# Kernel optimization log

Measured on AMD Instinct MI355X. Metric: run time of the kernel, lower is better.

The kernel has to match this reference:

```python
import jax, jax.numpy as jnp
import numpy as np

N_NODES = 50000
N_EDGES = 800000
EDGE_F = 96
NODE_F = 256
GLOB_F = 64
HIDDEN = 1024
N_GRAPHS = 8
MLP_IN = NODE_F + 3 * EDGE_F + GLOB_F  # 608


def setup_inputs() -> dict:
    key = jax.random.key(0)
    ks = jax.random.split(key, 9)
    x = jax.random.normal(ks[0], (N_NODES, NODE_F), dtype=jnp.float32)
    edge_attr = jax.random.normal(ks[1], (N_EDGES, EDGE_F), dtype=jnp.float32)
    u = jax.random.normal(ks[2], (N_GRAPHS, GLOB_F), dtype=jnp.float32)
    W1 = jax.random.normal(ks[3], (MLP_IN, HIDDEN), dtype=jnp.float32) * (1.0 / np.sqrt(MLP_IN))
    b1 = jax.random.normal(ks[4], (HIDDEN,), dtype=jnp.float32) * 0.01
    W2 = jax.random.normal(ks[5], (HIDDEN, NODE_F), dtype=jnp.float32) * (1.0 / np.sqrt(HIDDEN))
    b2 = jax.random.normal(ks[6], (NODE_F,), dtype=jnp.float32) * 0.01
    edge_index = jax.random.randint(ks[7], (2, N_EDGES), 0, N_NODES, dtype=jnp.int64 if jax.config.jax_enable_x64 else jnp.int32)
    batch = jnp.sort(jax.random.randint(ks[8], (N_NODES,), 0, N_GRAPHS, dtype=jnp.int32))
    return {"x": x, "edge_attr": edge_attr, "u": u, "W1": W1, "b1": b1,
            "W2": W2, "b2": b2, "edge_index": edge_index, "batch": batch}


def reference(x, edge_attr, u, W1, b1, W2, b2, edge_index, batch):
    col = edge_index[1]  # destination node for each edge
    n = x.shape[0]
    # sum / max / mean segment reductions over edges -> per-node features
    out1 = jax.ops.segment_sum(edge_attr, col, num_segments=n)                     # [N, E_F]
    cnt = jax.ops.segment_sum(jnp.ones((edge_attr.shape[0], 1), edge_attr.dtype), col, num_segments=n)  # [N,1]
    out2 = jax.ops.segment_max(edge_attr, col, num_segments=n)
    out2 = jnp.where(cnt > 0, out2, jnp.zeros_like(out2))  # torch_scatter gives 0 for empty segments
    out3 = out1 / jnp.maximum(cnt, 1.0)                    # mean; 0 for empty segments
    h = jnp.concatenate([x, out1, out2, out3, u[batch]], axis=1)  # [N, 608]
    h = jax.nn.relu(h @ W1 + b1) @ W2 + b2                        # node MLP
    return h + x  # residual
```

## Files before the change

kernel.cpp:

```cpp
#include <hip/hip_runtime.h>
#include <stdint.h>

#define N_NODES 50000
#define N_EDGES 800000
#define EDGE_F  96
#define NODE_F  256
#define GLOB_F  64
#define HIDDEN  1024
#define MLP_IN  608
#define KP      640
#define M_PAD   50176
#define SCAN_BLOCKS 196
#define NT1     10
#define NT2     16

typedef __bf16 bf16;
typedef __bf16 bf16x4 __attribute__((ext_vector_type(4)));
typedef __bf16 bf16x8 __attribute__((ext_vector_type(8)));
typedef float  f32x4  __attribute__((ext_vector_type(4)));

typedef __attribute__((address_space(1))) unsigned int gu32;
typedef __attribute__((address_space(3))) unsigned int lu32;

__device__ __forceinline__ void glds16(const void* g, void* l) {
    __builtin_amdgcn_global_load_lds((const gu32*)g, (lu32*)l, 16, 0, 0);
}

static constexpr size_t H_OFF    = 0;
static constexpr size_t H_BYTES  = (size_t)M_PAD * KP * 2;
static constexpr size_t HID_OFF  = H_OFF + H_BYTES;
static constexpr size_t HID_BYTES= (size_t)M_PAD * HIDDEN * 2;
static constexpr size_t W1T_OFF  = HID_OFF + HID_BYTES;
static constexpr size_t W1T_BYTES= (size_t)HIDDEN * KP * 2;
static constexpr size_t W2T_OFF  = W1T_OFF + W1T_BYTES;
static constexpr size_t W2T_BYTES= (size_t)NODE_F * HIDDEN * 2;
static constexpr size_t DEG_OFF  = W2T_OFF + W2T_BYTES;
static constexpr size_t DEG_BYTES= 200192;
static constexpr size_t CUR_OFF  = DEG_OFF + DEG_BYTES;
static constexpr size_t CUR_BYTES= 200192;
static constexpr size_t START_OFF= CUR_OFF + CUR_BYTES;
static constexpr size_t START_BYTES = 200192;
static constexpr size_t EIDS_OFF = START_OFF + START_BYTES;
static constexpr size_t EIDS_BYTES = (size_t)N_EDGES * 4;
static constexpr size_t BSUM_OFF = EIDS_OFF + EIDS_BYTES;
static constexpr size_t BSUM_BYTES = 1024;
static constexpr size_t BOFF_OFF = BSUM_OFF + BSUM_BYTES;

__global__ __launch_bounds__(256) void hist_kernel(const int* __restrict__ col,
                                                   int* __restrict__ deg) {
    int e = blockIdx.x * 256 + threadIdx.x;
    if (e < N_EDGES) atomicAdd(&deg[col[e]], 1);
}

__global__ __launch_bounds__(256) void scan_phase1(const int* __restrict__ deg,
                                                   int* __restrict__ start,
                                                   int* __restrict__ bsum) {
    __shared__ int sc[256];
    const int t = threadIdx.x, b = blockIdx.x;
    const int idx = b * 256 + t;
    int v = (idx < N_NODES) ? deg[idx] : 0;
    sc[t] = v;
    __syncthreads();
    for (int off = 1; off < 256; off <<= 1) {
        int add = (t >= off) ? sc[t - off] : 0;
        __syncthreads();
        sc[t] += add;
        __syncthreads();
    }
    if (idx < N_NODES) start[idx] = sc[t] - v;
    if (t == 255) bsum[b] = sc[255];
}

__global__ __launch_bounds__(256) void scan_phase2(int* __restrict__ bsum,
                                                   int* __restrict__ boff,
                                                   int* __restrict__ start) {
    __shared__ int sc[256];
    const int t = threadIdx.x;
    int v = (t < SCAN_BLOCKS) ? bsum[t] : 0;
    sc[t] = v;
    __syncthreads();
    for (int off = 1; off < 256; off <<= 1) {
        int add = (t >= off) ? sc[t - off] : 0;
        __syncthreads();
        sc[t] += add;
        __syncthreads();
    }
    if (t < SCAN_BLOCKS) boff[t] = sc[t] - v;
    if (t == 255) start[N_NODES] = sc[255];
}


__global__ __launch_bounds__(256) void scatter_kernel(const int* __restrict__ col,
                                                      const int* __restrict__ start,
                                                      const int* __restrict__ boff,
                                                      int* __restrict__ cursor,
                                                      int* __restrict__ eids) {
    int e = blockIdx.x * 256 + threadIdx.x;
    if (e < N_EDGES) {
        int c = col[e];
        int p = start[c] + boff[c >> 8] + atomicAdd(&cursor[c], 1);
        eids[p] = e;
    }
}

#define BH_CHUNK 128
__global__ __launch_bounds__(128) void build_h_kernel(const float* __restrict__ x,
                                                      const float* __restrict__ edge_attr,
                                                      const float* __restrict__ u,
                                                      const int* __restrict__ batch,
                                                      const int* __restrict__ start,
                                                      const int* __restrict__ boff,
                                                      const int* __restrict__ eids,
                                                      bf16* __restrict__ H) {
    const int n = blockIdx.x;
    const int t = threadIdx.x;
    bf16* row = H + (size_t)n * KP;
    if (n >= N_NODES) {
        for (int c = t; c < KP; c += 128) row[c] = (bf16)0.0f;
        return;
    }
    if (t < 64) {
        float4 v = ((const float4*)(x + (size_t)n * NODE_F))[t];
        bf16x4 p;
        p.x = (bf16)v.x; p.y = (bf16)v.y; p.z = (bf16)v.z; p.w = (bf16)v.w;
        *(bf16x4*)(row + t * 4) = p;
    } else {
        int g = batch[n];
        row[544 + (t - 64)] = (bf16)u[g * GLOB_F + (t - 64)];
    }
    if (t >= 96) row[608 + (t - 96)] = (bf16)0.0f;

    __shared__ int se[BH_CHUNK];
    __shared__ float4 red[96];
    const int s0 = start[n] + boff[n >> 8];
    const int s1 = (n == N_NODES - 1) ? N_EDGES
                                      : (start[n + 1] + boff[(n + 1) >> 8]);

    const int slot = t / 24;
    const int f4   = t - slot * 24;

    float4 sm4; sm4.x = 0.0f; sm4.y = 0.0f; sm4.z = 0.0f; sm4.w = 0.0f;
    float4 mx4; mx4.x = -3.0e38f; mx4.y = -3.0e38f; mx4.z = -3.0e38f; mx4.w = -3.0e38f;

#define ACC4(v) do { \
    sm4.x += (v).x; sm4.y += (v).y; sm4.z += (v).z; sm4.w += (v).w; \
    mx4.x = fmaxf(mx4.x, (v).x); mx4.y = fmaxf(mx4.y, (v).y); \
    mx4.z = fmaxf(mx4.z, (v).z); mx4.w = fmaxf(mx4.w, (v).w); \
} while (0)

    for (int base = s0; base < s1; base += BH_CHUNK) {
        const int cnt = min(BH_CHUNK, s1 - base);
        __syncthreads();
        if (t < cnt) se[t] = eids[base + t];
        __syncthreads();
        if (t < 96) {
            int i = 0;
            for (; i + 8 <= cnt; i += 8) {
                float4 v0 = *(const float4*)(edge_attr + (size_t)se[i + slot]     * EDGE_F + f4 * 4);
                float4 v1 = *(const float4*)(edge_attr + (size_t)se[i + 4 + slot] * EDGE_F + f4 * 4);
                ACC4(v0);
                ACC4(v1);
            }
            for (; i + 4 <= cnt; i += 4) {
                float4 v0 = *(const float4*)(edge_attr + (size_t)se[i + slot] * EDGE_F + f4 * 4);
                ACC4(v0);
            }
            if (slot == 0) {
                for (int k = i; k < cnt; ++k) {
                    float4 v0 = *(const float4*)(edge_attr + (size_t)se[k] * EDGE_F + f4 * 4);
                    ACC4(v0);
                }
            }
        }
    }
#undef ACC4

    __syncthreads();
    if (t < 96) red[t] = sm4;
    __syncthreads();
    float4 rs;
    if (t < 24) {
        float4 a0 = red[t], a1 = red[t + 24], a2 = red[t + 48], a3 = red[t + 72];
        rs.x = (a0.x + a1.x) + (a2.x + a3.x);
        rs.y = (a0.y + a1.y) + (a2.y + a3.y);
        rs.z = (a0.z + a1.z) + (a2.z + a3.z);
        rs.w = (a0.w + a1.w) + (a2.w + a3.w);
    }
    __syncthreads();
    if (t < 96) red[t] = mx4;
    __syncthreads();
    if (t < 24) {
        float4 a0 = red[t], a1 = red[t + 24], a2 = red[t + 48], a3 = red[t + 72];
        float4 rm;
        rm.x = fmaxf(fmaxf(a0.x, a1.x), fmaxf(a2.x, a3.x));
        rm.y = fmaxf(fmaxf(a0.y, a1.y), fmaxf(a2.y, a3.y));
        rm.z = fmaxf(fmaxf(a0.z, a1.z), fmaxf(a2.z, a3.z));
        rm.w = fmaxf(fmaxf(a0.w, a1.w), fmaxf(a2.w, a3.w));
        const int d = s1 - s0;
        if (d == 0) { rm.x = 0.0f; rm.y = 0.0f; rm.z = 0.0f; rm.w = 0.0f; }
        const float inv = 1.0f / fmaxf((float)d, 1.0f);
        bf16x4 ps, pm, pa;
        ps.x = (bf16)rs.x; ps.y = (bf16)rs.y; ps.z = (bf16)rs.z; ps.w = (bf16)rs.w;
        pm.x = (bf16)rm.x; pm.y = (bf16)rm.y; pm.z = (bf16)rm.z; pm.w = (bf16)rm.w;
        pa.x = (bf16)(rs.x * inv); pa.y = (bf16)(rs.y * inv);
        pa.z = (bf16)(rs.z * inv); pa.w = (bf16)(rs.w * inv);
        *(bf16x4*)(row + 256 + t * 4) = ps;
        *(bf16x4*)(row + 352 + t * 4) = pm;
        *(bf16x4*)(row + 448 + t * 4) = pa;
    }
}

__global__ __launch_bounds__(256) void transpose_kernel(const float* __restrict__ W,
                                                        bf16* __restrict__ Wt,
                                                        int K, int N, int Kpad) {
    __shared__ float tile[32][33];
    const int tx = threadIdx.x & 31, ty = threadIdx.x >> 5;
    const int n0 = blockIdx.x * 32, k0 = blockIdx.y * 32;
    if (k0 < K) {
#pragma unroll
        for (int r = 0; r < 4; r++)
            tile[ty + 8 * r][tx] = W[(size_t)(k0 + ty + 8 * r) * N + (n0 + tx)];
    }
    __syncthreads();
#pragma unroll
    for (int r = 0; r < 4; r++)
        Wt[(size_t)(n0 + ty + 8 * r) * Kpad + (k0 + tx)] =
            (k0 < K) ? (bf16)tile[tx][ty + 8 * r] : (bf16)0.0f;
}

#define VMC(n) asm volatile("s_waitcnt vmcnt(" #n ")" ::: "memory")
#define LGK0   asm volatile("s_waitcnt lgkmcnt(0)" ::: "memory")
#define BARR   __builtin_amdgcn_s_barrier()

__global__ __launch_bounds__(512) void gemm1_kernel(const bf16* __restrict__ H,
                                                    const bf16* __restrict__ Wt,
                                                    const float* __restrict__ b1,
                                                    bf16* __restrict__ hid) {
    __shared__ __align__(16) bf16 As[2][256 * 64];
    __shared__ __align__(16) bf16 Bs[2][256 * 64];
    const int t = threadIdx.x;
    const int wave = t >> 6, lane = t & 63;
    const int quad = lane >> 4, l16 = lane & 15;
    const int wr = wave >> 2;
    const int wc = wave & 3;
    const int orig = blockIdx.x;
    const int swz  = (orig & 7) * 98 + (orig >> 3);
    const int bm = swz >> 2, bn = swz & 3;

    f32x4 acc[8][4] = {};
    bf16x8 a[4][2], b[2][2];

    const int srow = t >> 3;
    const int scb  = (((t & 7) ^ (srow & 7)) << 4);
    const char* Ag = (const char*)H  + (size_t)(bm * 256) * (KP * 2);
    const char* Bg = (const char*)Wt + (size_t)(bn * 256) * (KP * 2);
    char* AsB = (char*)&As[0][0];
    char* BsB = (char*)&Bs[0][0];

    const int swzl = (l16 & 7) << 4;
    const int col0 = (quad * 16) ^ swzl;
    const int col1 = (64 + quad * 16) ^ swzl;

#define STG_A(buf, h, kt) do { \
    const char* _s = Ag + (size_t)((h) * 128) * (KP * 2) + (size_t)(kt) * 128; \
    char* _d = AsB + (buf) * 32768 + (h) * 16384 + t * 16; \
    glds16(_s + (size_t)srow * (KP * 2) + scb, _d); \
    glds16(_s + (size_t)(srow + 64) * (KP * 2) + scb, _d + 8192); \
} while (0)
#define STG_B(buf, h, kt) do { \
    const char* _s = Bg + (size_t)((h) * 128) * (KP * 2) + (size_t)(kt) * 128; \
    char* _d = BsB + (buf) * 32768 + (h) * 16384 + t * 16; \
    glds16(_s + (size_t)srow * (KP * 2) + scb, _d); \
    glds16(_s + (size_t)(srow + 64) * (KP * 2) + scb, _d + 8192); \
} while (0)
#define LDA(cbase, mq) do { \
    _Pragma("unroll") for (int i = 0; i < 4; ++i) { \
        const char* _p = (cbase) + (size_t)((mq) * 128 + wr * 64 + i * 16 + l16) * 128; \
        a[i][0] = *(const bf16x8*)(_p + col0); \
        a[i][1] = *(const bf16x8*)(_p + col1); \
    } } while (0)
#define LDB(cbase, nq) do { \
    _Pragma("unroll") for (int j = 0; j < 2; ++j) { \
        const char* _p = (cbase) + (size_t)((nq) * 128 + wc * 32 + j * 16 + l16) * 128; \
        b[j][0] = *(const bf16x8*)(_p + col0); \
        b[j][1] = *(const bf16x8*)(_p + col1); \
    } } while (0)
#define MMAQ(mq, nq) do { \
    __builtin_amdgcn_s_setprio(1); \
    _Pragma("unroll") for (int i = 0; i < 4; ++i) \
    _Pragma("unroll") for (int j = 0; j < 2; ++j) { \
        acc[(mq)*4+i][(nq)*2+j] = __builtin_amdgcn_mfma_f32_16x16x32_bf16(a[i][0], b[j][0], acc[(mq)*4+i][(nq)*2+j], 0, 0, 0); \
        acc[(mq)*4+i][(nq)*2+j] = __builtin_amdgcn_mfma_f32_16x16x32_bf16(a[i][1], b[j][1], acc[(mq)*4+i][(nq)*2+j], 0, 0, 0); \
    } \
    __builtin_amdgcn_s_setprio(0); \
} while (0)

    STG_A(0, 0, 0);
    STG_B(0, 0, 0);
    STG_B(0, 1, 0);
    STG_A(0, 1, 0);
    VMC(4);
    BARR;

#pragma unroll 1
    for (int kt = 0; kt < NT1 - 1; ++kt) {
        const int c = kt & 1, o = c ^ 1;
        const char* Ac = AsB + c * 32768;
        const char* Bc = BsB + c * 32768;
        LDA(Ac, 0); LDB(Bc, 0);
        STG_A(o, 0, kt + 1);
        VMC(4); BARR; LGK0;
        MMAQ(0, 0); BARR;
        LDB(Bc, 1);
        STG_B(o, 0, kt + 1);
        VMC(4); BARR; LGK0;
        MMAQ(0, 1); BARR;
        LDA(Ac, 1);
        STG_B(o, 1, kt + 1);
        BARR; LGK0;
        MMAQ(1, 1); BARR;
        LDB(Bc, 0);
        STG_A(o, 1, kt + 1);
        VMC(4); BARR; LGK0;
        MMAQ(1, 0); BARR;
    }
    {
        const int c = (NT1 - 1) & 1;
        const char* Ac = AsB + c * 32768;
        const char* Bc = BsB + c * 32768;
        LDA(Ac, 0); LDB(Bc, 0); VMC(2); BARR; LGK0; MMAQ(0, 0); BARR;
        LDB(Bc, 1);             VMC(0); BARR; LGK0; MMAQ(0, 1); BARR;
        LDA(Ac, 1);                     BARR; LGK0; MMAQ(1, 1); BARR;
        LDB(Bc, 0);                           LGK0; MMAQ(1, 0);
    }

#pragma unroll
    for (int m = 0; m < 8; ++m) {
        const int mq = m >> 2, i = m & 3;
        const int row0 = bm * 256 + mq * 128 + wr * 64 + i * 16 + quad * 4;
#pragma unroll
        for (int n = 0; n < 4; ++n) {
            const int nq = n >> 1, j = n & 1;
            const int col = bn * 256 + nq * 128 + wc * 32 + j * 16 + l16;
            const float bias = b1[col];
#pragma unroll
            for (int r = 0; r < 4; ++r) {
                float v = acc[m][n][r] + bias;
                v = fmaxf(v, 0.0f);
                hid[(size_t)(row0 + r) * HIDDEN + col] = (bf16)v;
            }
        }
    }
#undef STG_A
#undef STG_B
#undef LDA
#undef LDB
#undef MMAQ
}

__global__ __launch_bounds__(512) void gemm2_kernel(const bf16* __restrict__ Hd,
                                                    const bf16* __restrict__ Wt,
                                                    const float* __restrict__ b2,
                                                    const float* __restrict__ x,
                                                    float* __restrict__ out) {
    __shared__ __align__(16) bf16 As[2][256 * 64];
    __shared__ __align__(16) bf16 Bs[2][256 * 64];
    const int t = threadIdx.x;
    const int wave = t >> 6, lane = t & 63;
    const int quad = lane >> 4, l16 = lane & 15;
    const int wr = wave >> 2;
    const int wc = wave & 3;
    const int bm = blockIdx.x;

    f32x4 acc[8][4] = {};
    bf16x8 a[4][2], b[2][2];

    const int srow = t >> 3;
    const int scb  = (((t & 7) ^ (srow & 7)) << 4);
    const char* Ag = (const char*)Hd + (size_t)(bm * 256) * (HIDDEN * 2);
    const char* Bg = (const char*)Wt;
    char* AsB = (char*)&As[0][0];
    char* BsB = (char*)&Bs[0][0];

    const int swzl = (l16 & 7) << 4;
    const int col0 = (quad * 16) ^ swzl;
    const int col1 = (64 + quad * 16) ^ swzl;

#define STG_A2(buf, h, kt) do { \
    const char* _s = Ag + (size_t)((h) * 128) * (HIDDEN * 2) + (size_t)(kt) * 128; \
    char* _d = AsB + (buf) * 32768 + (h) * 16384 + t * 16; \
    glds16(_s + (size_t)srow * (HIDDEN * 2) + scb, _d); \
    glds16(_s + (size_t)(srow + 64) * (HIDDEN * 2) + scb, _d + 8192); \
} while (0)
#define STG_B2(buf, h, kt) do { \
    const char* _s = Bg + (size_t)((h) * 128) * (HIDDEN * 2) + (size_t)(kt) * 128; \
    char* _d = BsB + (buf) * 32768 + (h) * 16384 + t * 16; \
    glds16(_s + (size_t)srow * (HIDDEN * 2) + scb, _d); \
    glds16(_s + (size_t)(srow + 64) * (HIDDEN * 2) + scb, _d + 8192); \
} while (0)
#define LDA2(cbase, mq) do { \
    _Pragma("unroll") for (int i = 0; i < 4; ++i) { \
        const char* _p = (cbase) + (size_t)((mq) * 128 + wr * 64 + i * 16 + l16) * 128; \
        a[i][0] = *(const bf16x8*)(_p + col0); \
        a[i][1] = *(const bf16x8*)(_p + col1); \
    } } while (0)
#define LDB2(cbase, nq) do { \
    _Pragma("unroll") for (int j = 0; j < 2; ++j) { \
        const char* _p = (cbase) + (size_t)((nq) * 128 + wc * 32 + j * 16 + l16) * 128; \
        b[j][0] = *(const bf16x8*)(_p + col0); \
        b[j][1] = *(const bf16x8*)(_p + col1); \
    } } while (0)
#define MMAQ2(mq, nq) do { \
    __builtin_amdgcn_s_setprio(1); \
    _Pragma("unroll") for (int i = 0; i < 4; ++i) \
    _Pragma("unroll") for (int j = 0; j < 2; ++j) { \
        acc[(mq)*4+i][(nq)*2+j] = __builtin_amdgcn_mfma_f32_16x16x32_bf16(a[i][0], b[j][0], acc[(mq)*4+i][(nq)*2+j], 0, 0, 0); \
        acc[(mq)*4+i][(nq)*2+j] = __builtin_amdgcn_mfma_f32_16x16x32_bf16(a[i][1], b[j][1], acc[(mq)*4+i][(nq)*2+j], 0, 0, 0); \
    } \
    __builtin_amdgcn_s_setprio(0); \
} while (0)

    STG_A2(0, 0, 0);
    STG_B2(0, 0, 0);
    STG_B2(0, 1, 0);
    STG_A2(0, 1, 0);
    VMC(4);
    BARR;

#pragma unroll 1
    for (int kt = 0; kt < NT2 - 1; ++kt) {
        const int c = kt & 1, o = c ^ 1;
        const char* Ac = AsB + c * 32768;
        const char* Bc = BsB + c * 32768;
        LDA2(Ac, 0); LDB2(Bc, 0);
        STG_A2(o, 0, kt + 1);
        VMC(4); BARR; LGK0;
        MMAQ2(0, 0); BARR;
        LDB2(Bc, 1);
        STG_B2(o, 0, kt + 1);
        VMC(4); BARR; LGK0;
        MMAQ2(0, 1); BARR;
        LDA2(Ac, 1);
        STG_B2(o, 1, kt + 1);
        BARR; LGK0;
        MMAQ2(1, 1); BARR;
        LDB2(Bc, 0);
        STG_A2(o, 1, kt + 1);
        VMC(4); BARR; LGK0;
        MMAQ2(1, 0); BARR;
    }
    {
        const int c = (NT2 - 1) & 1;
        const char* Ac = AsB + c * 32768;
        const char* Bc = BsB + c * 32768;
        LDA2(Ac, 0); LDB2(Bc, 0); VMC(2); BARR; LGK0; MMAQ2(0, 0); BARR;
        LDB2(Bc, 1);              VMC(0); BARR; LGK0; MMAQ2(0, 1); BARR;
        LDA2(Ac, 1);                      BARR; LGK0; MMAQ2(1, 1); BARR;
        LDB2(Bc, 0);                            LGK0; MMAQ2(1, 0);
    }

#pragma unroll
    for (int m = 0; m < 8; ++m) {
        const int mq = m >> 2, i = m & 3;
        const int row0 = bm * 256 + mq * 128 + wr * 64 + i * 16 + quad * 4;
#pragma unroll
        for (int n = 0; n < 4; ++n) {
            const int nq = n >> 1, j = n & 1;
            const int col = nq * 128 + wc * 32 + j * 16 + l16;
            const float bias = b2[col];
#pragma unroll
            for (int r = 0; r < 4; ++r) {
                const int row = row0 + r;
                if (row < N_NODES) {
                    const size_t idx = (size_t)row * NODE_F + col;
                    out[idx] = acc[m][n][r] + bias + x[idx];
                }
            }
        }
    }
#undef STG_A2
#undef STG_B2
#undef LDA2
#undef LDB2
#undef MMAQ2
}

extern "C" void kernel_launch(void* const* d_in, const int* in_sizes, int n_in,
                              void* d_out, int out_size, void* d_ws, size_t ws_size,
                              hipStream_t stream) {
    const float* x         = (const float*)d_in[0];
    const float* edge_attr = (const float*)d_in[1];
    const float* u         = (const float*)d_in[2];
    const float* W1        = (const float*)d_in[3];
    const float* b1        = (const float*)d_in[4];
    const float* W2        = (const float*)d_in[5];
    const float* b2        = (const float*)d_in[6];
    const int*   edge_index= (const int*)d_in[7];
    const int*   batch     = (const int*)d_in[8];
    float*       out       = (float*)d_out;

    char* ws = (char*)d_ws;
    bf16* H    = (bf16*)(ws + H_OFF);
    bf16* hid  = (bf16*)(ws + HID_OFF);
    bf16* W1t  = (bf16*)(ws + W1T_OFF);
    bf16* W2t  = (bf16*)(ws + W2T_OFF);
    int*  deg  = (int*)(ws + DEG_OFF);
    int*  cur  = (int*)(ws + CUR_OFF);
    int*  start= (int*)(ws + START_OFF);
    int*  eids = (int*)(ws + EIDS_OFF);
    int*  bsum = (int*)(ws + BSUM_OFF);
    int*  boff = (int*)(ws + BOFF_OFF);

    const int* col = edge_index + N_EDGES;

    hipMemsetAsync(ws + DEG_OFF, 0, DEG_BYTES + CUR_BYTES, stream);
    hist_kernel<<<(N_EDGES + 255) / 256, 256, 0, stream>>>(col, deg);
    scan_phase1<<<SCAN_BLOCKS, 256, 0, stream>>>(deg, start, bsum);
    scan_phase2<<<1, 256, 0, stream>>>(bsum, boff, start);
    scatter_kernel<<<(N_EDGES + 255) / 256, 256, 0, stream>>>(col, start, boff, cur, eids);
    build_h_kernel<<<M_PAD, 128, 0, stream>>>(x, edge_attr, u, batch, start, boff, eids, H);
    transpose_kernel<<<dim3(HIDDEN / 32, KP / 32), 256, 0, stream>>>(W1, W1t, MLP_IN, HIDDEN, KP);
    transpose_kernel<<<dim3(NODE_F / 32, HIDDEN / 32), 256, 0, stream>>>(W2, W2t, HIDDEN, NODE_F, HIDDEN);
    gemm1_kernel<<<dim3(784), 512, 0, stream>>>(H, W1t, b1, hid);
    gemm2_kernel<<<dim3(196), 512, 0, stream>>>(hid, W2t, b2, x, out);
}
```

Measured before the change: 752.2 us.

## Record atomic ranks in histogram, merge transposes, unroll edge gather deeper

The histogram kernel now stores each edge's atomic return value as its rank, so the scatter pass writes eids directly with no second round of atomics. This also drops the cursor array and shrinks the memset. The two weight transposes become one launch, and the edge-gather loop in build_h loads four float4 per iteration instead of two for more memory-level parallelism. In exchange it writes and reads an extra 3.2MB rank array.

```diff
diff --git a/kernel.cpp b/kernel.cpp
--- a/kernel.cpp
+++ b/kernel.cpp
@@ -36,20 +36,21 @@
 static constexpr size_t W2T_BYTES= (size_t)NODE_F * HIDDEN * 2;
 static constexpr size_t DEG_OFF  = W2T_OFF + W2T_BYTES;
 static constexpr size_t DEG_BYTES= 200192;
-static constexpr size_t CUR_OFF  = DEG_OFF + DEG_BYTES;
-static constexpr size_t CUR_BYTES= 200192;
-static constexpr size_t START_OFF= CUR_OFF + CUR_BYTES;
+static constexpr size_t START_OFF= DEG_OFF + DEG_BYTES;
 static constexpr size_t START_BYTES = 200192;
 static constexpr size_t EIDS_OFF = START_OFF + START_BYTES;
 static constexpr size_t EIDS_BYTES = (size_t)N_EDGES * 4;
-static constexpr size_t BSUM_OFF = EIDS_OFF + EIDS_BYTES;
+static constexpr size_t RANK_OFF = EIDS_OFF + EIDS_BYTES;
+static constexpr size_t RANK_BYTES = (size_t)N_EDGES * 4;
+static constexpr size_t BSUM_OFF = RANK_OFF + RANK_BYTES;
 static constexpr size_t BSUM_BYTES = 1024;
 static constexpr size_t BOFF_OFF = BSUM_OFF + BSUM_BYTES;
 
-__global__ __launch_bounds__(256) void hist_kernel(const int* __restrict__ col,
-                                                   int* __restrict__ deg) {
+__global__ __launch_bounds__(256) void hist_rank_kernel(const int* __restrict__ col,
+                                                        int* __restrict__ deg,
+                                                        int* __restrict__ rank) {
     int e = blockIdx.x * 256 + threadIdx.x;
-    if (e < N_EDGES) atomicAdd(&deg[col[e]], 1);
+    if (e < N_EDGES) rank[e] = atomicAdd(&deg[col[e]], 1);
 }
 
 __global__ __launch_bounds__(256) void scan_phase1(const int* __restrict__ deg,
@@ -89,17 +90,15 @@
     if (t == 255) start[N_NODES] = sc[255];
 }
 
-
-__global__ __launch_bounds__(256) void scatter_kernel(const int* __restrict__ col,
-                                                      const int* __restrict__ start,
-                                                      const int* __restrict__ boff,
-                                                      int* __restrict__ cursor,
-                                                      int* __restrict__ eids) {
+__global__ __launch_bounds__(256) void place_kernel(const int* __restrict__ col,
+                                                    const int* __restrict__ start,
+                                                    const int* __restrict__ boff,
+                                                    const int* __restrict__ rank,
+                                                    int* __restrict__ eids) {
     int e = blockIdx.x * 256 + threadIdx.x;
     if (e < N_EDGES) {
         int c = col[e];
-        int p = start[c] + boff[c >> 8] + atomicAdd(&cursor[c], 1);
-        eids[p] = e;
+        eids[start[c] + boff[c >> 8] + rank[e]] = e;
     }
 }
 
@@ -155,11 +154,12 @@
         __syncthreads();
         if (t < 96) {
             int i = 0;
-            for (; i + 8 <= cnt; i += 8) {
-                float4 v0 = *(const float4*)(edge_attr + (size_t)se[i + slot]     * EDGE_F + f4 * 4);
-                float4 v1 = *(const float4*)(edge_attr + (size_t)se[i + 4 + slot] * EDGE_F + f4 * 4);
-                ACC4(v0);
-                ACC4(v1);
+            for (; i + 16 <= cnt; i += 16) {
+                float4 v0 = *(const float4*)(edge_attr + (size_t)se[i + slot]      * EDGE_F + f4 * 4);
+                float4 v1 = *(const float4*)(edge_attr + (size_t)se[i + 4 + slot]  * EDGE_F + f4 * 4);
+                float4 v2 = *(const float4*)(edge_attr + (size_t)se[i + 8 + slot]  * EDGE_F + f4 * 4);
+                float4 v3 = *(const float4*)(edge_attr + (size_t)se[i + 12 + slot] * EDGE_F + f4 * 4);
+                ACC4(v0); ACC4(v1); ACC4(v2); ACC4(v3);
             }
             for (; i + 4 <= cnt; i += 4) {
                 float4 v0 = *(const float4*)(edge_attr + (size_t)se[i + slot] * EDGE_F + f4 * 4);
@@ -210,12 +210,22 @@
     }
 }
 
-__global__ __launch_bounds__(256) void transpose_kernel(const float* __restrict__ W,
-                                                        bf16* __restrict__ Wt,
-                                                        int K, int N, int Kpad) {
+__global__ __launch_bounds__(256) void transpose2_kernel(const float* __restrict__ W1,
+                                                         bf16* __restrict__ W1t,
+                                                         const float* __restrict__ W2,
+                                                         bf16* __restrict__ W2t) {
     __shared__ float tile[32][33];
     const int tx = threadIdx.x & 31, ty = threadIdx.x >> 5;
-    const int n0 = blockIdx.x * 32, k0 = blockIdx.y * 32;
+    int bid = blockIdx.x;
+    const float* W; bf16* Wt; int K, N, Kpad, n0, k0;
+    if (bid < 640) {
+        W = W1; Wt = (bf16*)W1t; K = MLP_IN; N = HIDDEN; Kpad = KP;
+        n0 = (bid & 31) * 32; k0 = (bid >> 5) * 32;
+    } else {
+        bid -= 640;
+        W = W2; Wt = (bf16*)W2t; K = HIDDEN; N = NODE_F; Kpad = HIDDEN;
+        n0 = (bid & 7) * 32; k0 = (bid >> 3) * 32;
+    }
     if (k0 < K) {
 #pragma unroll
         for (int r = 0; r < 4; r++)
@@ -505,22 +515,21 @@
     bf16* W1t  = (bf16*)(ws + W1T_OFF);
     bf16* W2t  = (bf16*)(ws + W2T_OFF);
     int*  deg  = (int*)(ws + DEG_OFF);
-    int*  cur  = (int*)(ws + CUR_OFF);
     int*  start= (int*)(ws + START_OFF);
     int*  eids = (int*)(ws + EIDS_OFF);
+    int*  rank = (int*)(ws + RANK_OFF);
     int*  bsum = (int*)(ws + BSUM_OFF);
     int*  boff = (int*)(ws + BOFF_OFF);
 
     const int* col = edge_index + N_EDGES;
 
-    hipMemsetAsync(ws + DEG_OFF, 0, DEG_BYTES + CUR_BYTES, stream);
-    hist_kernel<<<(N_EDGES + 255) / 256, 256, 0, stream>>>(col, deg);
+    hipMemsetAsync(ws + DEG_OFF, 0, DEG_BYTES, stream);
+    hist_rank_kernel<<<(N_EDGES + 255) / 256, 256, 0, stream>>>(col, deg, rank);
     scan_phase1<<<SCAN_BLOCKS, 256, 0, stream>>>(deg, start, bsum);
     scan_phase2<<<1, 256, 0, stream>>>(bsum, boff, start);
-    scatter_kernel<<<(N_EDGES + 255) / 256, 256, 0, stream>>>(col, start, boff, cur, eids);
+    place_kernel<<<(N_EDGES + 255) / 256, 256, 0, stream>>>(col, start, boff, rank, eids);
     build_h_kernel<<<M_PAD, 128, 0, stream>>>(x, edge_attr, u, batch, start, boff, eids, H);
-    transpose_kernel<<<dim3(HIDDEN / 32, KP / 32), 256, 0, stream>>>(W1, W1t, MLP_IN, HIDDEN, KP);
-    transpose_kernel<<<dim3(NODE_F / 32, HIDDEN / 32), 256, 0, stream>>>(W2, W2t, HIDDEN, NODE_F, HIDDEN);
+    transpose2_kernel<<<896, 256, 0, stream>>>(W1, W1t, W2, W2t);
     gemm1_kernel<<<dim3(784), 512, 0, stream>>>(H, W1t, b1, hid);
     gemm2_kernel<<<dim3(196), 512, 0, stream>>>(hid, W2t, b2, x, out);
 }
```

New measurement: 733.2 us. -2.5%, faster.
